# Performance work log

Hardware: AMD Instinct MI355X
Metric: run time of the kernel (lower is better)

Reference implementation:

```python
import jax, jax.numpy as jnp
import numpy as np
from jax import lax

B, T, D, NH = 8, 2048, 128, 4
HD = D // NH
EPS = 1e-5


def _ln(x, g, b):
    m = x.mean(-1, keepdims=True)
    v = ((x - m) ** 2).mean(-1, keepdims=True)
    return (x - m) / jnp.sqrt(v + EPS) * g + b


def _gelu(x):  # exact (erf) GELU, matching torch nn.GELU default
    return jax.nn.gelu(x, approximate=False)


def _forward(lob_feat, trade_feat, has_trade,
             ei_w, ei_b, ei_g, ei_beta, decay,
             in_proj_w, in_proj_b, out_proj_w, out_proj_b,
             cn_g, cn_b,
             lob_w, lob_b, lob_g, lob_beta,
             tr_w, tr_b, tr_g, tr_beta,
             of_w, of_b, of_g, of_beta):
    # event impact: Linear -> LayerNorm -> Tanh, gated by has_trade
    impact = jnp.tanh(_ln(trade_feat @ ei_w.T + ei_b, ei_g, ei_beta))
    impact = impact * has_trade[..., None]              # [B,T,D]

    # diagonal linear recurrence: state_t = sigmoid(decay) * state_{t-1} + impact_t
    d = jax.nn.sigmoid(decay)                           # [D]

    def step(s, x):
        s = d * s + x
        return s, s

    _, states = lax.scan(step, jnp.zeros_like(impact[:, 0]),
                         jnp.swapaxes(impact, 0, 1))    # [T,B,D]
    state_seq = jnp.swapaxes(states, 0, 1)              # [B,T,D]

    # fusion MLPs (dropout is identity in eval)
    lob_enh = _gelu(_ln(jnp.concatenate([lob_feat, state_seq], -1) @ lob_w.T + lob_b,
                        lob_g, lob_beta))
    trade_enh = _gelu(_ln(jnp.concatenate([trade_feat, state_seq], -1) @ tr_w.T + tr_b,
                          tr_g, tr_beta))

    # torch nn.MultiheadAttention (batch_first): q=lob_enh, k=v=trade_enh
    wq, wk, wv = in_proj_w[:D], in_proj_w[D:2 * D], in_proj_w[2 * D:]
    bq, bk, bv = in_proj_b[:D], in_proj_b[D:2 * D], in_proj_b[2 * D:]
    q = (lob_enh @ wq.T + bq).reshape(B, T, NH, HD)
    k = (trade_enh @ wk.T + bk).reshape(B, T, NH, HD)
    v = (trade_enh @ wv.T + bv).reshape(B, T, NH, HD)
    scores = jnp.einsum('bqhd,bkhd->bhqk', q, k) / jnp.sqrt(jnp.float32(HD))
    attn = jax.nn.softmax(scores, axis=-1)
    ctx = jnp.einsum('bhqk,bkhd->bqhd', attn, v).reshape(B, T, D)
    fused_attn = ctx @ out_proj_w.T + out_proj_b

    fused = _ln(lob_enh + fused_attn, cn_g, cn_b)
    output = _gelu(_ln(jnp.concatenate([fused, trade_enh], -1) @ of_w.T + of_b,
                       of_g, of_beta))
    return output


def setup_inputs() -> dict:
    key = jax.random.key(0)
    ks = jax.random.split(key, 20)
    s1 = 1.0 / np.sqrt(D)
    s2 = 1.0 / np.sqrt(2 * D)
    return {
        'lob_feat': jax.random.normal(ks[0], (B, T, D), jnp.float32),
        'trade_feat': jax.random.normal(ks[1], (B, T, D), jnp.float32),
        'has_trade': (jax.random.uniform(ks[2], (B, T)) < 0.5).astype(jnp.float32),
        'ei_w': jax.random.normal(ks[3], (D, D), jnp.float32) * s1,
        'ei_b': jnp.zeros((D,), jnp.float32),
        'ei_g': jnp.ones((D,), jnp.float32),
        'ei_beta': jnp.zeros((D,), jnp.float32),
        'decay': jnp.ones((D,), jnp.float32) * 0.9,
        'in_proj_w': jax.random.normal(ks[4], (3 * D, D), jnp.float32) * s1,
        'in_proj_b': jnp.zeros((3 * D,), jnp.float32),
        'out_proj_w': jax.random.normal(ks[5], (D, D), jnp.float32) * s1,
        'out_proj_b': jnp.zeros((D,), jnp.float32),
        'cn_g': jnp.ones((D,), jnp.float32),
        'cn_b': jnp.zeros((D,), jnp.float32),
        'lob_w': jax.random.normal(ks[6], (D, 2 * D), jnp.float32) * s2,
        'lob_b': jnp.zeros((D,), jnp.float32),
        'lob_g': jnp.ones((D,), jnp.float32),
        'lob_beta': jnp.zeros((D,), jnp.float32),
        'tr_w': jax.random.normal(ks[7], (D, 2 * D), jnp.float32) * s2,
        'tr_b': jnp.zeros((D,), jnp.float32),
        'tr_g': jnp.ones((D,), jnp.float32),
        'tr_beta': jnp.zeros((D,), jnp.float32),
        'of_w': jax.random.normal(ks[8], (D, 2 * D), jnp.float32) * s2,
        'of_b': jnp.zeros((D,), jnp.float32),
        'of_g': jnp.ones((D,), jnp.float32),
        'of_beta': jnp.zeros((D,), jnp.float32),
    }


def reference(lob_feat, trade_feat, has_trade,
              ei_w, ei_b, ei_g, ei_beta, decay,
              in_proj_w, in_proj_b, out_proj_w, out_proj_b,
              cn_g, cn_b,
              lob_w, lob_b, lob_g, lob_beta,
              tr_w, tr_b, tr_g, tr_beta,
              of_w, of_b, of_g, of_beta):
    return _forward(lob_feat, trade_feat, has_trade,
                    ei_w, ei_b, ei_g, ei_beta, decay,
                    in_proj_w, in_proj_b, out_proj_w, out_proj_b,
                    cn_g, cn_b,
                    lob_w, lob_b, lob_g, lob_beta,
                    tr_w, tr_b, tr_g, tr_beta,
                    of_w, of_b, of_g, of_beta)
```

## Files before the change

### kernel.cpp

```cpp
#include <hip/hip_runtime.h>
#include <math.h>


#define T_  2048

typedef short bf16x8 __attribute__((ext_vector_type(8)));
typedef float f32x4  __attribute__((ext_vector_type(4)));
typedef unsigned short ushort_t;

__device__ __forceinline__ float sigm(float x) { return 1.0f / (1.0f + __expf(-x)); }

__device__ __forceinline__ unsigned short f2bf(float x) {
    union { float f; unsigned u; } v; v.f = x;
    unsigned r = v.u + 0x7FFFu + ((v.u >> 16) & 1u);
    return (unsigned short)(r >> 16);
}

__device__ __forceinline__ float gelu_f(float x) {
    const float e = exp2f(fmaf(0.044715f * x, x * x, x) * -2.3022083f);
    return x * __builtin_amdgcn_rcpf(1.0f + e);
}
__device__ __forceinline__ float tanh_f(float y) {
    const float e = exp2f(y * 2.8853900818f);
    return 1.0f - 2.0f * __builtin_amdgcn_rcpf(e + 1.0f);
}

__global__ __launch_bounds__(256) void prep_kernel(
    const float* __restrict__ lob, const float* __restrict__ trade,
    const float* __restrict__ eiw, const float* __restrict__ ipw,
    const float* __restrict__ opw, const float* __restrict__ lobw,
    const float* __restrict__ trw, const float* __restrict__ ofw,
    ushort_t* __restrict__ pool)
{
    const size_t i8 = ((size_t)blockIdx.x * 256 + threadIdx.x) * 8;
    const float* src; size_t off;
    if      (i8 < 2097152) { src = lob;   off = 0; }
    else if (i8 < 4194304) { src = trade; off = 2097152; }
    else if (i8 < 4210688) { src = eiw;   off = 4194304; }
    else if (i8 < 4259840) { src = ipw;   off = 4210688; }
    else if (i8 < 4276224) { src = opw;   off = 4259840; }
    else if (i8 < 4308992) { src = lobw;  off = 4276224; }
    else if (i8 < 4341760) { src = trw;   off = 4308992; }
    else                   { src = ofw;   off = 4341760; }
    const float4 a = *(const float4*)(src + (i8 - off));
    const float4 b = *(const float4*)(src + (i8 - off) + 4);
    bf16x8 o;
    o[0] = (short)f2bf(a.x); o[1] = (short)f2bf(a.y);
    o[2] = (short)f2bf(a.z); o[3] = (short)f2bf(a.w);
    o[4] = (short)f2bf(b.x); o[5] = (short)f2bf(b.y);
    o[6] = (short)f2bf(b.z); o[7] = (short)f2bf(b.w);
    *(bf16x8*)(pool + i8) = o;
}

__global__ __launch_bounds__(256) void gemm_ei(
    const ushort_t* __restrict__ Xb0, const ushort_t* __restrict__ Wb,
    const float* __restrict__ bias, const float* __restrict__ gamma,
    const float* __restrict__ beta, const float* __restrict__ extra,
    float* __restrict__ outf)
{
    __shared__ float red[32][2][2];
    const int tid = threadIdx.x, wid = tid >> 6, lane = tid & 63;
    const int c2 = lane & 15, g = lane >> 4;
    const int rowblk = wid >> 1, chf = wid & 1, cb0 = chf * 4;
    const int R0 = blockIdx.x * 32 + rowblk * 16;

    f32x4 acc[4] = {};
#pragma unroll
    for (int ch = 0; ch < 4; ch++) {
        const bf16x8 a = *(const bf16x8*)(Xb0 + (size_t)(R0 + c2) * 128 + ch * 32 + g * 8);
#pragma unroll
        for (int j = 0; j < 4; j++) {
            const bf16x8 b = *(const bf16x8*)(Wb + (size_t)((cb0 + j) * 16 + c2) * 128 + ch * 32 + g * 8);
            acc[j] = __builtin_amdgcn_mfma_f32_16x16x32_bf16(a, b, acc[j], 0, 0, 0);
        }
    }
    float gm[4], bt[4];
#pragma unroll
    for (int j = 0; j < 4; j++) {
        const int col = (cb0 + j) * 16 + c2;
        const float bb = bias[col];
        gm[j] = gamma[col]; bt[j] = beta[col];
#pragma unroll
        for (int r = 0; r < 4; r++) acc[j][r] += bb;
    }
#pragma unroll
    for (int r = 0; r < 4; r++) {
        float s = 0.f, ss = 0.f;
#pragma unroll
        for (int j = 0; j < 4; j++) { const float v = acc[j][r]; s += v; ss = fmaf(v, v, ss); }
#pragma unroll
        for (int o = 8; o; o >>= 1) { s += __shfl_xor(s, o); ss += __shfl_xor(ss, o); }
        if (c2 == 0) {
            red[rowblk * 16 + 4 * g + r][chf][0] = s;
            red[rowblk * 16 + 4 * g + r][chf][1] = ss;
        }
    }
    __syncthreads();
#pragma unroll
    for (int r = 0; r < 4; r++) {
        const int lr = rowblk * 16 + 4 * g + r;
        const float S  = red[lr][0][0] + red[lr][1][0];
        const float SS = red[lr][0][1] + red[lr][1][1];
        const float mean = S * (1.0f / 128.0f);
        float var = SS * (1.0f / 128.0f) - mean * mean;
        var = fmaxf(var, 0.0f);
        const float rstd = rsqrtf(var + 1e-5f);
        const int R = blockIdx.x * 32 + lr;
        const float ext = extra[R];
#pragma unroll
        for (int j = 0; j < 4; j++) {
            const float y = (acc[j][r] - mean) * rstd * gm[j] + bt[j];
            outf[(size_t)R * 128 + (cb0 + j) * 16 + c2] = tanh_f(y) * ext;
        }
    }
}

__global__ __launch_bounds__(256) void enh_qkv(
    const ushort_t* __restrict__ lobb, const ushort_t* __restrict__ trab,
    const ushort_t* __restrict__ stab,
    const ushort_t* __restrict__ lobw, const ushort_t* __restrict__ trw,
    const ushort_t* __restrict__ ipw, const float* __restrict__ ipb,
    const float* __restrict__ lob_b, const float* __restrict__ lob_g,
    const float* __restrict__ lob_beta,
    const float* __restrict__ tr_b, const float* __restrict__ tr_g,
    const float* __restrict__ tr_beta,
    float* __restrict__ lobe_f, ushort_t* __restrict__ tre_bf,
    ushort_t* __restrict__ qo, ushort_t* __restrict__ ko, ushort_t* __restrict__ vo)
{
    __shared__ ushort_t lob_t[32][136];
    __shared__ ushort_t tre_t[32][136];
    __shared__ ushort_t vls[128][36];
    __shared__ float red[32][2][4];
    const int tid = threadIdx.x, wid = tid >> 6, lane = tid & 63;
    const int c2 = lane & 15, g = lane >> 4;
    const int rowblk = wid >> 1, chf = wid & 1, cb0 = chf * 4;
    const int RB = blockIdx.x * 32;
    const int R0 = RB + rowblk * 16;

    f32x4 aL[4] = {}, aT[4] = {};
#pragma unroll
    for (int ch = 0; ch < 8; ch++) {
        const int kk = (ch & 3) * 32;
        bf16x8 xl, xt;
        if (ch < 4) {
            xl = *(const bf16x8*)(lobb + (size_t)(R0 + c2) * 128 + kk + g * 8);
            xt = *(const bf16x8*)(trab + (size_t)(R0 + c2) * 128 + kk + g * 8);
        } else {
            xl = *(const bf16x8*)(stab + (size_t)(R0 + c2) * 128 + kk + g * 8);
            xt = xl;
        }
#pragma unroll
        for (int j = 0; j < 4; j++) {
            const size_t wo = (size_t)((cb0 + j) * 16 + c2) * 256 + ch * 32 + g * 8;
            aL[j] = __builtin_amdgcn_mfma_f32_16x16x32_bf16(xl, *(const bf16x8*)(lobw + wo), aL[j], 0, 0, 0);
            aT[j] = __builtin_amdgcn_mfma_f32_16x16x32_bf16(xt, *(const bf16x8*)(trw + wo), aT[j], 0, 0, 0);
        }
    }
#pragma unroll
    for (int j = 0; j < 4; j++) {
        const int col = (cb0 + j) * 16 + c2;
        const float bL = lob_b[col], bT = tr_b[col];
#pragma unroll
        for (int r = 0; r < 4; r++) { aL[j][r] += bL; aT[j][r] += bT; }
    }
#pragma unroll
    for (int r = 0; r < 4; r++) {
        float sL = 0.f, ssL = 0.f, sT = 0.f, ssT = 0.f;
#pragma unroll
        for (int j = 0; j < 4; j++) {
            const float vL = aL[j][r], vT = aT[j][r];
            sL += vL; ssL = fmaf(vL, vL, ssL);
            sT += vT; ssT = fmaf(vT, vT, ssT);
        }
#pragma unroll
        for (int o = 8; o; o >>= 1) {
            sL += __shfl_xor(sL, o); ssL += __shfl_xor(ssL, o);
            sT += __shfl_xor(sT, o); ssT += __shfl_xor(ssT, o);
        }
        if (c2 == 0) {
            float* rd = red[rowblk * 16 + 4 * g + r][chf];
            rd[0] = sL; rd[1] = ssL; rd[2] = sT; rd[3] = ssT;
        }
    }
    __syncthreads();
#pragma unroll
    for (int r = 0; r < 4; r++) {
        const int lr = rowblk * 16 + 4 * g + r;
        const int R = RB + lr;
        const float SL  = red[lr][0][0] + red[lr][1][0];
        const float SSL = red[lr][0][1] + red[lr][1][1];
        const float ST  = red[lr][0][2] + red[lr][1][2];
        const float SST = red[lr][0][3] + red[lr][1][3];
        const float mL = SL * (1.0f / 128.0f), mT = ST * (1.0f / 128.0f);
        const float rL = rsqrtf(fmaxf(SSL * (1.0f / 128.0f) - mL * mL, 0.0f) + 1e-5f);
        const float rT = rsqrtf(fmaxf(SST * (1.0f / 128.0f) - mT * mT, 0.0f) + 1e-5f);
#pragma unroll
        for (int j = 0; j < 4; j++) {
            const int col = (cb0 + j) * 16 + c2;
            const float yL = gelu_f((aL[j][r] - mL) * rL * lob_g[col] + lob_beta[col]);
            const float yT = gelu_f((aT[j][r] - mT) * rT * tr_g[col] + tr_beta[col]);
            lobe_f[(size_t)R * 128 + col] = yL;
            lob_t[lr][col] = f2bf(yL);
            const ushort_t tb = f2bf(yT);
            tre_bf[(size_t)R * 128 + col] = tb;
            tre_t[lr][col] = tb;
        }
    }
    __syncthreads();

    const float qscale = 0.17677669529663687f * 1.4426950408889634f;
#pragma unroll
    for (int which = 0; which < 3; which++) {
        const ushort_t (*src)[136] = (which == 0) ? lob_t : tre_t;
        const ushort_t* Wp = ipw + (size_t)which * 16384;
        f32x4 pa[4] = {};
#pragma unroll
        for (int ch = 0; ch < 4; ch++) {
            const bf16x8 a = *(const bf16x8*)&src[rowblk * 16 + c2][ch * 32 + g * 8];
#pragma unroll
            for (int j = 0; j < 4; j++) {
                const bf16x8 b = *(const bf16x8*)(Wp + (size_t)((cb0 + j) * 16 + c2) * 128 + ch * 32 + g * 8);
                pa[j] = __builtin_amdgcn_mfma_f32_16x16x32_bf16(a, b, pa[j], 0, 0, 0);
            }
        }
        if (which < 2) {
            ushort_t* dst = (which == 0) ? qo : ko;
            const float sc = (which == 0) ? qscale : 1.0f;
#pragma unroll
            for (int j = 0; j < 4; j++) {
                const int col = (cb0 + j) * 16 + c2;
                const float bb = ipb[which * 128 + col];
                const int h = col >> 5, hd = col & 31;
#pragma unroll
                for (int r = 0; r < 4; r++) {
                    const int R = R0 + 4 * g + r;
                    const int b = R >> 11, t = R & 2047;
                    dst[(((size_t)b * 4 + h) * 2048 + t) * 32 + hd] = f2bf((pa[j][r] + bb) * sc);
                }
            }
        } else {
#pragma unroll
            for (int j = 0; j < 4; j++) {
                const int col = (cb0 + j) * 16 + c2;
                const float bb = ipb[256 + col];
#pragma unroll
                for (int r = 0; r < 4; r++)
                    vls[col][rowblk * 16 + 4 * g + r] = f2bf(pa[j][r] + bb);
            }
        }
    }
    __syncthreads();
    {
        const int col = tid >> 1, hf = tid & 1;
        const int h = col >> 5, hd = col & 31;
        const int b = RB >> 11;
        unsigned w[8];
#pragma unroll
        for (int e = 0; e < 8; e++) {
            const int cp = hf * 8 + e;
            w[e] = (unsigned)vls[col][cp] | ((unsigned)vls[col][cp + 16] << 16);
        }
        ushort_t* dst = vo + (((size_t)b * 4 + h) * 32 + hd) * 2048 + (RB & 2047) + hf * 16;
        *(uint4*)dst       = *(const uint4*)&w[0];
        *(uint4*)(dst + 8) = *(const uint4*)&w[4];
    }
}

__global__ __launch_bounds__(256) void attn_kernel(
    const ushort_t* __restrict__ q, const ushort_t* __restrict__ k,
    const ushort_t* __restrict__ vtg, ushort_t* __restrict__ ctx)
{
    __shared__ ushort_t ks[2][64][40];
    __shared__ ushort_t vt[2][32][72];
    __shared__ ushort_t ps[64][72];
    const int tid = threadIdx.x, wid = tid >> 6, lane = tid & 63;
    const int c = lane & 15, g = lane >> 4;
    const int qt = blockIdx.x, bh = blockIdx.y, b = bh >> 2, h = bh & 3;
    const ushort_t* kb_ = k   + (size_t)bh * 65536;
    const ushort_t* vb_ = vtg + (size_t)bh * 65536;

    const bf16x8 qf = *(const bf16x8*)(q + ((size_t)bh * 2048 + qt * 64 + wid * 16 + c) * 32 + g * 8);

    float m_i[4], rs_[4];
    f32x4 acc[2] = {};
#pragma unroll
    for (int r = 0; r < 4; r++) { m_i[r] = 8.0f; rs_[r] = 0.0f; }

    const int srow = tid >> 2, ssg = tid & 3;
    const int vd = tid >> 3, vkg = tid & 7;

    {
        const bf16x8 kk8 = *(const bf16x8*)(kb_ + (size_t)srow * 32 + ssg * 8);
        const bf16x8 vv8 = *(const bf16x8*)(vb_ + (size_t)vd * 2048 + vkg * 8);
        *(bf16x8*)&ks[0][srow][ssg * 8] = kk8;
        *(bf16x8*)&vt[0][vd][vkg * 8] = vv8;
    }
    __syncthreads();

    for (int kt = 0; kt < 32; kt++) {
        const int cur = kt & 1;
        bf16x8 kk8, vv8;
        if (kt + 1 < 32) {
            kk8 = *(const bf16x8*)(kb_ + ((size_t)(kt + 1) * 64 + srow) * 32 + ssg * 8);
            vv8 = *(const bf16x8*)(vb_ + (size_t)vd * 2048 + (kt + 1) * 64 + vkg * 8);
        }

        f32x4 s[4];
        __builtin_amdgcn_s_setprio(1);
#pragma unroll
        for (int kb2 = 0; kb2 < 4; kb2++) {
            const bf16x8 kf = *(const bf16x8*)&ks[cur][kb2 * 16 + c][g * 8];
            f32x4 z = {};
            s[kb2] = __builtin_amdgcn_mfma_f32_16x16x32_bf16(qf, kf, z, 0, 0, 0);
        }
        __builtin_amdgcn_s_setprio(0);

        int need = 0;
        float lmax[4];
#pragma unroll
        for (int r = 0; r < 4; r++) {
            lmax[r] = fmaxf(fmaxf(s[0][r], s[1][r]), fmaxf(s[2][r], s[3][r]));
            need |= (lmax[r] > m_i[r] + 40.0f) ? 1 : 0;
        }
        if (__any(need)) {
#pragma unroll
            for (int r = 0; r < 4; r++) {
                float tm = lmax[r];
#pragma unroll
                for (int o = 8; o; o >>= 1) tm = fmaxf(tm, __shfl_xor(tm, o));
                const float mn = fmaxf(m_i[r], tm);
                const float al = exp2f(m_i[r] - mn);
                rs_[r] *= al; acc[0][r] *= al; acc[1][r] *= al;
                m_i[r] = mn;
            }
        }

#pragma unroll
        for (int r = 0; r < 4; r++) {
            const float p0 = exp2f(s[0][r] - m_i[r]);
            const float p1 = exp2f(s[1][r] - m_i[r]);
            const float p2 = exp2f(s[2][r] - m_i[r]);
            const float p3 = exp2f(s[3][r] - m_i[r]);
            rs_[r] += (p0 + p1) + (p2 + p3);
            unsigned w01, w23;
            asm("v_cvt_pk_bf16_f32 %0, %1, %2" : "=v"(w01) : "v"(p0), "v"(p1));
            asm("v_cvt_pk_bf16_f32 %0, %1, %2" : "=v"(w23) : "v"(p2), "v"(p3));
            ushort_t* prow = ps[wid * 16 + 4 * g + r];
            *(unsigned*)&prow[2 * c] = w01;
            *(unsigned*)&prow[32 + 2 * c] = w23;
        }

        const bf16x8 pa0 = *(const bf16x8*)&ps[wid * 16 + c][g * 8];
        const bf16x8 pa1 = *(const bf16x8*)&ps[wid * 16 + c][32 + g * 8];
        __builtin_amdgcn_s_setprio(1);
#pragma unroll
        for (int nb = 0; nb < 2; nb++) {
            const bf16x8 v0 = *(const bf16x8*)&vt[cur][nb * 16 + c][g * 8];
            const bf16x8 v1 = *(const bf16x8*)&vt[cur][nb * 16 + c][32 + g * 8];
            acc[nb] = __builtin_amdgcn_mfma_f32_16x16x32_bf16(pa0, v0, acc[nb], 0, 0, 0);
            acc[nb] = __builtin_amdgcn_mfma_f32_16x16x32_bf16(pa1, v1, acc[nb], 0, 0, 0);
        }
        __builtin_amdgcn_s_setprio(0);

        if (kt + 1 < 32) {
            *(bf16x8*)&ks[cur ^ 1][srow][ssg * 8] = kk8;
            *(bf16x8*)&vt[cur ^ 1][vd][vkg * 8] = vv8;
        }
        __syncthreads();
    }

#pragma unroll
    for (int r = 0; r < 4; r++) {
        float t = rs_[r];
#pragma unroll
        for (int o = 8; o; o >>= 1) t += __shfl_xor(t, o);
        const float inv = __builtin_amdgcn_rcpf(t);
        const int tq = qt * 64 + wid * 16 + 4 * g + r;
        ushort_t* dst = ctx + ((size_t)(b * 2048 + tq)) * 128 + h * 32;
        dst[c]      = f2bf(acc[0][r] * inv);
        dst[16 + c] = f2bf(acc[1][r] * inv);
    }
}

__global__ __launch_bounds__(256) void out_fuse(
    const ushort_t* __restrict__ ctxb, const ushort_t* __restrict__ treb,
    const ushort_t* __restrict__ opw, const float* __restrict__ opb,
    const float* __restrict__ cn_g, const float* __restrict__ cn_b,
    const ushort_t* __restrict__ ofw, const float* __restrict__ of_b,
    const float* __restrict__ of_g, const float* __restrict__ of_beta,
    const float* __restrict__ lobe_f, float* __restrict__ out)
{
    __shared__ ushort_t fus_t[32][136];
    __shared__ float red[32][2][2];
    const int tid = threadIdx.x, wid = tid >> 6, lane = tid & 63;
    const int c2 = lane & 15, g = lane >> 4;
    const int rowblk = wid >> 1, chf = wid & 1, cb0 = chf * 4;
    const int RB = blockIdx.x * 32;
    const int R0 = RB + rowblk * 16;

    f32x4 acc[4] = {};
#pragma unroll
    for (int ch = 0; ch < 4; ch++) {
        const bf16x8 a = *(const bf16x8*)(ctxb + (size_t)(R0 + c2) * 128 + ch * 32 + g * 8);
#pragma unroll
        for (int j = 0; j < 4; j++) {
            const bf16x8 b = *(const bf16x8*)(opw + (size_t)((cb0 + j) * 16 + c2) * 128 + ch * 32 + g * 8);
            acc[j] = __builtin_amdgcn_mfma_f32_16x16x32_bf16(a, b, acc[j], 0, 0, 0);
        }
    }
#pragma unroll
    for (int j = 0; j < 4; j++) {
        const int col = (cb0 + j) * 16 + c2;
        const float bb = opb[col];
#pragma unroll
        for (int r = 0; r < 4; r++)
            acc[j][r] += bb + lobe_f[(size_t)(R0 + 4 * g + r) * 128 + col];
    }
#pragma unroll
    for (int r = 0; r < 4; r++) {
        float s = 0.f, ss = 0.f;
#pragma unroll
        for (int j = 0; j < 4; j++) { const float v = acc[j][r]; s += v; ss = fmaf(v, v, ss); }
#pragma unroll
        for (int o = 8; o; o >>= 1) { s += __shfl_xor(s, o); ss += __shfl_xor(ss, o); }
        if (c2 == 0) {
            red[rowblk * 16 + 4 * g + r][chf][0] = s;
            red[rowblk * 16 + 4 * g + r][chf][1] = ss;
        }
    }
    __syncthreads();
#pragma unroll
    for (int r = 0; r < 4; r++) {
        const int lr = rowblk * 16 + 4 * g + r;
        const float S  = red[lr][0][0] + red[lr][1][0];
        const float SS = red[lr][0][1] + red[lr][1][1];
        const float mean = S * (1.0f / 128.0f);
        const float rstd = rsqrtf(fmaxf(SS * (1.0f / 128.0f) - mean * mean, 0.0f) + 1e-5f);
#pragma unroll
        for (int j = 0; j < 4; j++) {
            const int col = (cb0 + j) * 16 + c2;
            fus_t[lr][col] = f2bf((acc[j][r] - mean) * rstd * cn_g[col] + cn_b[col]);
        }
    }
    __syncthreads();

    f32x4 a2[4] = {};
#pragma unroll
    for (int ch = 0; ch < 8; ch++) {
        bf16x8 a;
        if (ch < 4) a = *(const bf16x8*)&fus_t[rowblk * 16 + c2][ch * 32 + g * 8];
        else        a = *(const bf16x8*)(treb + (size_t)(R0 + c2) * 128 + (ch - 4) * 32 + g * 8);
#pragma unroll
        for (int j = 0; j < 4; j++) {
            const bf16x8 b = *(const bf16x8*)(ofw + (size_t)((cb0 + j) * 16 + c2) * 256 + ch * 32 + g * 8);
            a2[j] = __builtin_amdgcn_mfma_f32_16x16x32_bf16(a, b, a2[j], 0, 0, 0);
        }
    }
#pragma unroll
    for (int j = 0; j < 4; j++) {
        const float bb = of_b[(cb0 + j) * 16 + c2];
#pragma unroll
        for (int r = 0; r < 4; r++) a2[j][r] += bb;
    }
#pragma unroll
    for (int r = 0; r < 4; r++) {
        float s = 0.f, ss = 0.f;
#pragma unroll
        for (int j = 0; j < 4; j++) { const float v = a2[j][r]; s += v; ss = fmaf(v, v, ss); }
#pragma unroll
        for (int o = 8; o; o >>= 1) { s += __shfl_xor(s, o); ss += __shfl_xor(ss, o); }
        if (c2 == 0) {
            red[rowblk * 16 + 4 * g + r][chf][0] = s;
            red[rowblk * 16 + 4 * g + r][chf][1] = ss;
        }
    }
    __syncthreads();
#pragma unroll
    for (int r = 0; r < 4; r++) {
        const int lr = rowblk * 16 + 4 * g + r;
        const float S  = red[lr][0][0] + red[lr][1][0];
        const float SS = red[lr][0][1] + red[lr][1][1];
        const float mean = S * (1.0f / 128.0f);
        const float rstd = rsqrtf(fmaxf(SS * (1.0f / 128.0f) - mean * mean, 0.0f) + 1e-5f);
        const int R = RB + lr;
#pragma unroll
        for (int j = 0; j < 4; j++) {
            const int col = (cb0 + j) * 16 + c2;
            const float y = (a2[j][r] - mean) * rstd * of_g[col] + of_beta[col];
            out[(size_t)R * 128 + col] = gelu_f(y);
        }
    }
}

__global__ void scan_local_kernel(float* __restrict__ st, const float* __restrict__ decay)
{
    const int c = threadIdx.x;
    const int ch = blockIdx.x, b = blockIdx.y;
    const float d = sigm(decay[c]);
    const size_t base = ((size_t)b * T_ + ch * 64) * 128 + c;
    float s = 0.0f;
#pragma unroll 4
    for (int tl = 0; tl < 64; tl++) {
        const float x = st[base + (size_t)tl * 128];
        s = fmaf(d, s, x);
        st[base + (size_t)tl * 128] = s;
    }
}

__global__ void scan_carry_kernel(const float* __restrict__ st, const float* __restrict__ decay,
                                  float* __restrict__ carry)
{
    const int c = threadIdx.x;
    const int b = blockIdx.x;
    const float d = sigm(decay[c]);
    float dl = d;
#pragma unroll
    for (int i = 0; i < 6; i++) dl *= dl;
    float ends[32];
#pragma unroll
    for (int ch = 0; ch < 32; ch++)
        ends[ch] = st[((size_t)b * T_ + ch * 64 + 63) * 128 + c];
    float e = 0.0f;
#pragma unroll
    for (int ch = 0; ch < 32; ch++) {
        carry[((size_t)b * 32 + ch) * 128 + c] = e;
        e = fmaf(dl, e, ends[ch]);
    }
}

__global__ void scan_fin_kernel(const float* __restrict__ st, const float* __restrict__ decay,
                                const float* __restrict__ carry, ushort_t* __restrict__ stbf)
{
    const int c = threadIdx.x;
    const int ch = blockIdx.x, b = blockIdx.y;
    const float d = sigm(decay[c]);
    const float cr = ch ? carry[((size_t)b * 32 + ch) * 128 + c] : 0.0f;
    const size_t base = ((size_t)b * T_ + ch * 64) * 128 + c;
    float p = d;
#pragma unroll 4
    for (int tl = 0; tl < 64; tl++) {
        const float s2 = st[base + (size_t)tl * 128] + p * cr;
        p *= d;
        stbf[base + (size_t)tl * 128] = f2bf(s2);
    }
}

extern "C" void kernel_launch(void* const* d_in, const int* in_sizes, int n_in,
                              void* d_out, int out_size, void* d_ws, size_t ws_size,
                              hipStream_t stream)
{
    const float* lob_feat   = (const float*)d_in[0];
    const float* trade_feat = (const float*)d_in[1];
    const float* has_trade  = (const float*)d_in[2];
    const float* ei_w       = (const float*)d_in[3];
    const float* ei_b       = (const float*)d_in[4];
    const float* ei_g       = (const float*)d_in[5];
    const float* ei_beta    = (const float*)d_in[6];
    const float* decay      = (const float*)d_in[7];
    const float* in_proj_w  = (const float*)d_in[8];
    const float* in_proj_b  = (const float*)d_in[9];
    const float* out_proj_w = (const float*)d_in[10];
    const float* out_proj_b = (const float*)d_in[11];
    const float* cn_g       = (const float*)d_in[12];
    const float* cn_b       = (const float*)d_in[13];
    const float* lob_w      = (const float*)d_in[14];
    const float* lob_b      = (const float*)d_in[15];
    const float* lob_g      = (const float*)d_in[16];
    const float* lob_beta   = (const float*)d_in[17];
    const float* tr_w       = (const float*)d_in[18];
    const float* tr_b       = (const float*)d_in[19];
    const float* tr_g       = (const float*)d_in[20];
    const float* tr_beta    = (const float*)d_in[21];
    const float* of_w       = (const float*)d_in[22];
    const float* of_b       = (const float*)d_in[23];
    const float* of_g       = (const float*)d_in[24];
    const float* of_beta    = (const float*)d_in[25];

    char* W = (char*)d_ws;
    const size_t MB = 1u << 20;
    float*    state_f  = (float*)W;
    float*    lobe_f   = state_f;
    float*    carry    = (float*)(W + 8 * MB);
    ushort_t* pool     = (ushort_t*)(W + 9 * MB);
    ushort_t* state_bf = (ushort_t*)(W + 18 * MB);
    ushort_t* tre_bf   = (ushort_t*)(W + 26 * MB);
    ushort_t* q_bf     = (ushort_t*)(W + 30 * MB);
    ushort_t* k_bf     = (ushort_t*)(W + 34 * MB);
    ushort_t* vt_g     = (ushort_t*)(W + 38 * MB);
    ushort_t* ctx_bf   = (ushort_t*)(W + 42 * MB);

    ushort_t* lob_bf   = pool;
    ushort_t* trade_bf = pool + 2097152;
    ushort_t* eiw_bf   = pool + 4194304;
    ushort_t* ipw_bf   = pool + 4210688;
    ushort_t* opw_bf   = pool + 4259840;
    ushort_t* lobw_bf  = pool + 4276224;
    ushort_t* trw_bf   = pool + 4308992;
    ushort_t* ofw_bf   = pool + 4341760;

    const dim3 blk(256);

    prep_kernel<<<dim3(2136), blk, 0, stream>>>(lob_feat, trade_feat, ei_w, in_proj_w,
                                                out_proj_w, lob_w, tr_w, of_w, pool);
    gemm_ei<<<dim3(512), blk, 0, stream>>>(trade_bf, eiw_bf, ei_b, ei_g, ei_beta,
                                           has_trade, state_f);
    scan_local_kernel<<<dim3(32, 8), dim3(128), 0, stream>>>(state_f, decay);
    scan_carry_kernel<<<dim3(8), dim3(128), 0, stream>>>(state_f, decay, carry);
    scan_fin_kernel<<<dim3(32, 8), dim3(128), 0, stream>>>(state_f, decay, carry, state_bf);
    enh_qkv<<<dim3(512), blk, 0, stream>>>(lob_bf, trade_bf, state_bf, lobw_bf, trw_bf,
                                           ipw_bf, in_proj_b, lob_b, lob_g, lob_beta,
                                           tr_b, tr_g, tr_beta, lobe_f, tre_bf,
                                           q_bf, k_bf, vt_g);
    attn_kernel<<<dim3(32, 32), blk, 0, stream>>>(q_bf, k_bf, vt_g, ctx_bf);
    out_fuse<<<dim3(512), blk, 0, stream>>>(ctx_bf, tre_bf, opw_bf, out_proj_b, cn_g, cn_b,
                                            ofw_bf, of_b, of_g, of_beta, lobe_f, (float*)d_out);
}
```

Measured before the change: 149.4 us.

## Keep softmax probabilities in registers and store impact as bf16 for scan

The attention kernel now swaps the MFMA operand order so that scores come out transposed. Each lane then holds a full query column and can feed P straight into the PV MFMA as a register operand. This removes the LDS round trip for the probability tile and cuts the row-max and row-sum shuffles. The V transpose layout in enh_qkv is permuted to match, and the output store is vectorized. Separately, the event-impact result is written as bf16, and the scan is restructured into an ends/carry/recompute pass, which reduces fp32 state traffic at some precision cost in the recurrence input.

```diff
diff --git a/kernel.cpp b/kernel.cpp
--- a/kernel.cpp
+++ b/kernel.cpp
@@ -14,6 +14,9 @@
     union { float f; unsigned u; } v; v.f = x;
     unsigned r = v.u + 0x7FFFu + ((v.u >> 16) & 1u);
     return (unsigned short)(r >> 16);
+}
+__device__ __forceinline__ float bf2f(ushort_t u) {
+    union { unsigned u; float f; } v; v.u = ((unsigned)u) << 16; return v.f;
 }
 
 __device__ __forceinline__ float gelu_f(float x) {
@@ -56,7 +59,7 @@
     const ushort_t* __restrict__ Xb0, const ushort_t* __restrict__ Wb,
     const float* __restrict__ bias, const float* __restrict__ gamma,
     const float* __restrict__ beta, const float* __restrict__ extra,
-    float* __restrict__ outf)
+    ushort_t* __restrict__ outb)
 {
     __shared__ float red[32][2][2];
     const int tid = threadIdx.x, wid = tid >> 6, lane = tid & 63;
@@ -110,7 +113,7 @@
 #pragma unroll
         for (int j = 0; j < 4; j++) {
             const float y = (acc[j][r] - mean) * rstd * gm[j] + bt[j];
-            outf[(size_t)R * 128 + (cb0 + j) * 16 + c2] = tanh_f(y) * ext;
+            outb[(size_t)R * 128 + (cb0 + j) * 16 + c2] = f2bf(tanh_f(y) * ext);
         }
     }
 }
@@ -257,8 +260,10 @@
         unsigned w[8];
 #pragma unroll
         for (int e = 0; e < 8; e++) {
-            const int cp = hf * 8 + e;
-            w[e] = (unsigned)vls[col][cp] | ((unsigned)vls[col][cp + 16] << 16);
+            const int p0 = hf * 16 + 2 * e;
+            const int g2 = p0 >> 3, j2 = p0 & 7;
+            const int lk = 4 * g2 + j2 + (j2 >= 4 ? 12 : 0);
+            w[e] = (unsigned)vls[col][lk] | ((unsigned)vls[col][lk + 1] << 16);
         }
         ushort_t* dst = vo + (((size_t)b * 4 + h) * 32 + hd) * 2048 + (RB & 2047) + hf * 16;
         *(uint4*)dst       = *(const uint4*)&w[0];
@@ -272,7 +277,6 @@
 {
     __shared__ ushort_t ks[2][64][40];
     __shared__ ushort_t vt[2][32][72];
-    __shared__ ushort_t ps[64][72];
     const int tid = threadIdx.x, wid = tid >> 6, lane = tid & 63;
     const int c = lane & 15, g = lane >> 4;
     const int qt = blockIdx.x, bh = blockIdx.y, b = bh >> 2, h = bh & 3;
@@ -281,10 +285,8 @@
 
     const bf16x8 qf = *(const bf16x8*)(q + ((size_t)bh * 2048 + qt * 64 + wid * 16 + c) * 32 + g * 8);
 
-    float m_i[4], rs_[4];
+    float m_i = 8.0f, rs = 0.0f;
     f32x4 acc[2] = {};
-#pragma unroll
-    for (int r = 0; r < 4; r++) { m_i[r] = 8.0f; rs_[r] = 0.0f; }
 
     const int srow = tid >> 2, ssg = tid & 3;
     const int vd = tid >> 3, vkg = tid & 7;
@@ -311,54 +313,54 @@
         for (int kb2 = 0; kb2 < 4; kb2++) {
             const bf16x8 kf = *(const bf16x8*)&ks[cur][kb2 * 16 + c][g * 8];
             f32x4 z = {};
-            s[kb2] = __builtin_amdgcn_mfma_f32_16x16x32_bf16(qf, kf, z, 0, 0, 0);
+            s[kb2] = __builtin_amdgcn_mfma_f32_16x16x32_bf16(kf, qf, z, 0, 0, 0);
         }
         __builtin_amdgcn_s_setprio(0);
 
-        int need = 0;
-        float lmax[4];
-#pragma unroll
-        for (int r = 0; r < 4; r++) {
-            lmax[r] = fmaxf(fmaxf(s[0][r], s[1][r]), fmaxf(s[2][r], s[3][r]));
-            need |= (lmax[r] > m_i[r] + 40.0f) ? 1 : 0;
-        }
-        if (__any(need)) {
-#pragma unroll
-            for (int r = 0; r < 4; r++) {
-                float tm = lmax[r];
-#pragma unroll
-                for (int o = 8; o; o >>= 1) tm = fmaxf(tm, __shfl_xor(tm, o));
-                const float mn = fmaxf(m_i[r], tm);
-                const float al = exp2f(m_i[r] - mn);
-                rs_[r] *= al; acc[0][r] *= al; acc[1][r] *= al;
-                m_i[r] = mn;
-            }
-        }
-
-#pragma unroll
-        for (int r = 0; r < 4; r++) {
-            const float p0 = exp2f(s[0][r] - m_i[r]);
-            const float p1 = exp2f(s[1][r] - m_i[r]);
-            const float p2 = exp2f(s[2][r] - m_i[r]);
-            const float p3 = exp2f(s[3][r] - m_i[r]);
-            rs_[r] += (p0 + p1) + (p2 + p3);
-            unsigned w01, w23;
-            asm("v_cvt_pk_bf16_f32 %0, %1, %2" : "=v"(w01) : "v"(p0), "v"(p1));
-            asm("v_cvt_pk_bf16_f32 %0, %1, %2" : "=v"(w23) : "v"(p2), "v"(p3));
-            ushort_t* prow = ps[wid * 16 + 4 * g + r];
-            *(unsigned*)&prow[2 * c] = w01;
-            *(unsigned*)&prow[32 + 2 * c] = w23;
-        }
-
-        const bf16x8 pa0 = *(const bf16x8*)&ps[wid * 16 + c][g * 8];
-        const bf16x8 pa1 = *(const bf16x8*)&ps[wid * 16 + c][32 + g * 8];
+        float lm = s[0][0];
+#pragma unroll
+        for (int kb2 = 0; kb2 < 4; kb2++)
+#pragma unroll
+            for (int r = 0; r < 4; r++) lm = fmaxf(lm, s[kb2][r]);
+        if (__any(lm > m_i + 40.0f)) {
+            float tm = lm;
+            tm = fmaxf(tm, __shfl_xor(tm, 16));
+            tm = fmaxf(tm, __shfl_xor(tm, 32));
+            const float mn = fmaxf(m_i, tm);
+            const float al = exp2f(m_i - mn);
+            rs *= al;
+#pragma unroll
+            for (int nb = 0; nb < 2; nb++)
+#pragma unroll
+                for (int r = 0; r < 4; r++) acc[nb][r] *= al;
+            m_i = mn;
+        }
+
+#pragma unroll
+        for (int kb2 = 0; kb2 < 4; kb2++)
+#pragma unroll
+            for (int r = 0; r < 4; r++) s[kb2][r] = exp2f(s[kb2][r] - m_i);
+        rs += ((s[0][0] + s[0][1]) + (s[0][2] + s[0][3]))
+            + ((s[1][0] + s[1][1]) + (s[1][2] + s[1][3]))
+            + ((s[2][0] + s[2][1]) + (s[2][2] + s[2][3]))
+            + ((s[3][0] + s[3][1]) + (s[3][2] + s[3][3]));
+        union { unsigned u[4]; bf16x8 v; } pf0, pf1;
+        asm("v_cvt_pk_bf16_f32 %0, %1, %2" : "=v"(pf0.u[0]) : "v"(s[0][0]), "v"(s[0][1]));
+        asm("v_cvt_pk_bf16_f32 %0, %1, %2" : "=v"(pf0.u[1]) : "v"(s[0][2]), "v"(s[0][3]));
+        asm("v_cvt_pk_bf16_f32 %0, %1, %2" : "=v"(pf0.u[2]) : "v"(s[1][0]), "v"(s[1][1]));
+        asm("v_cvt_pk_bf16_f32 %0, %1, %2" : "=v"(pf0.u[3]) : "v"(s[1][2]), "v"(s[1][3]));
+        asm("v_cvt_pk_bf16_f32 %0, %1, %2" : "=v"(pf1.u[0]) : "v"(s[2][0]), "v"(s[2][1]));
+        asm("v_cvt_pk_bf16_f32 %0, %1, %2" : "=v"(pf1.u[1]) : "v"(s[2][2]), "v"(s[2][3]));
+        asm("v_cvt_pk_bf16_f32 %0, %1, %2" : "=v"(pf1.u[2]) : "v"(s[3][0]), "v"(s[3][1]));
+        asm("v_cvt_pk_bf16_f32 %0, %1, %2" : "=v"(pf1.u[3]) : "v"(s[3][2]), "v"(s[3][3]));
+
         __builtin_amdgcn_s_setprio(1);
 #pragma unroll
         for (int nb = 0; nb < 2; nb++) {
             const bf16x8 v0 = *(const bf16x8*)&vt[cur][nb * 16 + c][g * 8];
             const bf16x8 v1 = *(const bf16x8*)&vt[cur][nb * 16 + c][32 + g * 8];
-            acc[nb] = __builtin_amdgcn_mfma_f32_16x16x32_bf16(pa0, v0, acc[nb], 0, 0, 0);
-            acc[nb] = __builtin_amdgcn_mfma_f32_16x16x32_bf16(pa1, v1, acc[nb], 0, 0, 0);
+            acc[nb] = __builtin_amdgcn_mfma_f32_16x16x32_bf16(v0, pf0.v, acc[nb], 0, 0, 0);
+            acc[nb] = __builtin_amdgcn_mfma_f32_16x16x32_bf16(v1, pf1.v, acc[nb], 0, 0, 0);
         }
         __builtin_amdgcn_s_setprio(0);
 
@@ -369,16 +371,20 @@
         __syncthreads();
     }
 
-#pragma unroll
-    for (int r = 0; r < 4; r++) {
-        float t = rs_[r];
-#pragma unroll
-        for (int o = 8; o; o >>= 1) t += __shfl_xor(t, o);
-        const float inv = __builtin_amdgcn_rcpf(t);
-        const int tq = qt * 64 + wid * 16 + 4 * g + r;
-        ushort_t* dst = ctx + ((size_t)(b * 2048 + tq)) * 128 + h * 32;
-        dst[c]      = f2bf(acc[0][r] * inv);
-        dst[16 + c] = f2bf(acc[1][r] * inv);
+    rs += __shfl_xor(rs, 16);
+    rs += __shfl_xor(rs, 32);
+    const float inv = __builtin_amdgcn_rcpf(rs);
+    const int q_ = qt * 64 + wid * 16 + c;
+    ushort_t* dst = ctx + ((size_t)(b * 2048 + q_)) * 128 + h * 32;
+#pragma unroll
+    for (int nb = 0; nb < 2; nb++) {
+        unsigned w0, w1;
+        const float a0 = acc[nb][0] * inv, a1 = acc[nb][1] * inv;
+        const float a2 = acc[nb][2] * inv, a3 = acc[nb][3] * inv;
+        asm("v_cvt_pk_bf16_f32 %0, %1, %2" : "=v"(w0) : "v"(a0), "v"(a1));
+        asm("v_cvt_pk_bf16_f32 %0, %1, %2" : "=v"(w1) : "v"(a2), "v"(a3));
+        uint2 wv; wv.x = w0; wv.y = w1;
+        *(uint2*)(dst + nb * 16 + 4 * g) = wv;
     }
 }
 
@@ -492,7 +498,9 @@
     }
 }
 
-__global__ void scan_local_kernel(float* __restrict__ st, const float* __restrict__ decay)
+__global__ void scan_ends_kernel(const ushort_t* __restrict__ imp,
+                                 const float* __restrict__ decay,
+                                 float* __restrict__ ends)
 {
     const int c = threadIdx.x;
     const int ch = blockIdx.x, b = blockIdx.y;
@@ -500,14 +508,13 @@
     const size_t base = ((size_t)b * T_ + ch * 64) * 128 + c;
     float s = 0.0f;
 #pragma unroll 4
-    for (int tl = 0; tl < 64; tl++) {
-        const float x = st[base + (size_t)tl * 128];
-        s = fmaf(d, s, x);
-        st[base + (size_t)tl * 128] = s;
-    }
-}
-
-__global__ void scan_carry_kernel(const float* __restrict__ st, const float* __restrict__ decay,
+    for (int tl = 0; tl < 64; tl++)
+        s = fmaf(d, s, bf2f(imp[base + (size_t)tl * 128]));
+    ends[((size_t)b * 32 + ch) * 128 + c] = s;
+}
+
+__global__ void scan_carry_kernel(const float* __restrict__ ends,
+                                  const float* __restrict__ decay,
                                   float* __restrict__ carry)
 {
     const int c = threadIdx.x;
@@ -516,32 +523,28 @@
     float dl = d;
 #pragma unroll
     for (int i = 0; i < 6; i++) dl *= dl;
-    float ends[32];
-#pragma unroll
-    for (int ch = 0; ch < 32; ch++)
-        ends[ch] = st[((size_t)b * T_ + ch * 64 + 63) * 128 + c];
     float e = 0.0f;
 #pragma unroll
     for (int ch = 0; ch < 32; ch++) {
         carry[((size_t)b * 32 + ch) * 128 + c] = e;
-        e = fmaf(dl, e, ends[ch]);
-    }
-}
-
-__global__ void scan_fin_kernel(const float* __restrict__ st, const float* __restrict__ decay,
-                                const float* __restrict__ carry, ushort_t* __restrict__ stbf)
+        e = fmaf(dl, e, ends[((size_t)b * 32 + ch) * 128 + c]);
+    }
+}
+
+__global__ void scan_fin_kernel(const ushort_t* __restrict__ imp,
+                                const float* __restrict__ decay,
+                                const float* __restrict__ carry,
+                                ushort_t* __restrict__ stbf)
 {
     const int c = threadIdx.x;
     const int ch = blockIdx.x, b = blockIdx.y;
     const float d = sigm(decay[c]);
-    const float cr = ch ? carry[((size_t)b * 32 + ch) * 128 + c] : 0.0f;
+    float s = carry[((size_t)b * 32 + ch) * 128 + c];
     const size_t base = ((size_t)b * T_ + ch * 64) * 128 + c;
-    float p = d;
 #pragma unroll 4
     for (int tl = 0; tl < 64; tl++) {
-        const float s2 = st[base + (size_t)tl * 128] + p * cr;
-        p *= d;
-        stbf[base + (size_t)tl * 128] = f2bf(s2);
+        s = fmaf(d, s, bf2f(imp[base + (size_t)tl * 128]));
+        stbf[base + (size_t)tl * 128] = f2bf(s);
     }
 }
 
@@ -578,11 +581,12 @@
 
     char* W = (char*)d_ws;
     const size_t MB = 1u << 20;
-    float*    state_f  = (float*)W;
-    float*    lobe_f   = state_f;
+    float*    lobe_f   = (float*)W;
     float*    carry    = (float*)(W + 8 * MB);
+    float*    ends     = (float*)(W + 8 * MB + 256 * 1024);
     ushort_t* pool     = (ushort_t*)(W + 9 * MB);
-    ushort_t* state_bf = (ushort_t*)(W + 18 * MB);
+    ushort_t* imp_bf   = (ushort_t*)(W + 18 * MB);
+    ushort_t* state_bf = (ushort_t*)(W + 22 * MB);
     ushort_t* tre_bf   = (ushort_t*)(W + 26 * MB);
     ushort_t* q_bf     = (ushort_t*)(W + 30 * MB);
     ushort_t* k_bf     = (ushort_t*)(W + 34 * MB);
@@ -603,10 +607,10 @@
     prep_kernel<<<dim3(2136), blk, 0, stream>>>(lob_feat, trade_feat, ei_w, in_proj_w,
                                                 out_proj_w, lob_w, tr_w, of_w, pool);
     gemm_ei<<<dim3(512), blk, 0, stream>>>(trade_bf, eiw_bf, ei_b, ei_g, ei_beta,
-                                           has_trade, state_f);
-    scan_local_kernel<<<dim3(32, 8), dim3(128), 0, stream>>>(state_f, decay);
-    scan_carry_kernel<<<dim3(8), dim3(128), 0, stream>>>(state_f, decay, carry);
-    scan_fin_kernel<<<dim3(32, 8), dim3(128), 0, stream>>>(state_f, decay, carry, state_bf);
+                                           has_trade, imp_bf);
+    scan_ends_kernel<<<dim3(32, 8), dim3(128), 0, stream>>>(imp_bf, decay, ends);
+    scan_carry_kernel<<<dim3(8), dim3(128), 0, stream>>>(ends, decay, carry);
+    scan_fin_kernel<<<dim3(32, 8), dim3(128), 0, stream>>>(imp_bf, decay, carry, state_bf);
     enh_qkv<<<dim3(512), blk, 0, stream>>>(lob_bf, trade_bf, state_bf, lobw_bf, trw_bf,
                                            ipw_bf, in_proj_b, lob_b, lob_g, lob_beta,
                                            tr_b, tr_g, tr_beta, lobe_f, tre_bf,
```

Result: faster. 139.2 us (-6.8%).
